# Performance work log

Hardware: AMD Instinct MI355X
Metric: run time of the kernel (lower is better)

Reference implementation:

```python
import jax, jax.numpy as jnp
from jax import lax
import numpy as np

HH = WW = 128          # backbone feature map (2048px image / stride 16)
C_IN = 512
FEAT_STRIDE = 16
N_ANCHOR = 9
NMS_THRESH = 0.7
N_PRE_NMS = 6000
N_POST_NMS = 300
MIN_SIZE = 16
NEG = jnp.float32(-1e30)


def _anchor_base(base_size=16, ratios=(0.5, 1.0, 2.0), scales=(8, 16, 32)):
    py = px = base_size / 2.0
    ab = np.zeros((len(ratios) * len(scales), 4), np.float32)
    for i, r in enumerate(ratios):
        for j, s in enumerate(scales):
            h = base_size * s * np.sqrt(r)
            w = base_size * s * np.sqrt(1.0 / r)
            ab[i * len(scales) + j] = [py - h / 2, px - w / 2, py + h / 2, px + w / 2]
    return ab


def _shifted_anchors(hh, ww):
    # (y1, x1, y2, x2) anchors enumerated row-major over (y, x), anchors innermost
    ab = _anchor_base()
    sy = np.arange(0, hh * FEAT_STRIDE, FEAT_STRIDE, dtype=np.float32)
    sx = np.arange(0, ww * FEAT_STRIDE, FEAT_STRIDE, dtype=np.float32)
    sx, sy = np.meshgrid(sx, sy)
    shift = np.stack((sy.ravel(), sx.ravel(), sy.ravel(), sx.ravel()), axis=1)
    anc = (ab[None, :, :] + shift[:, None, :]).reshape(-1, 4)
    return jnp.asarray(anc)


def _conv(x, w, b):
    y = lax.conv_general_dilated(x, w, (1, 1), 'SAME',
                                 dimension_numbers=('NHWC', 'HWIO', 'NHWC'))
    return y + b


def _loc2bbox(anchor, loc):
    sh = anchor[:, 2] - anchor[:, 0]
    sw = anchor[:, 3] - anchor[:, 1]
    scy = anchor[:, 0] + 0.5 * sh
    scx = anchor[:, 1] + 0.5 * sw
    cy = loc[:, 0] * sh + scy
    cx = loc[:, 1] * sw + scx
    h = jnp.exp(loc[:, 2]) * sh
    w = jnp.exp(loc[:, 3]) * sw
    return jnp.stack([cy - 0.5 * h, cx - 0.5 * w, cy + 0.5 * h, cx + 0.5 * w], axis=1)


def _nms(boxes, scores, thresh, n_out):
    # Greedy NMS with a fixed output size; invalid slots are zeroed.
    y1, x1, y2, x2 = boxes[:, 0], boxes[:, 1], boxes[:, 2], boxes[:, 3]
    areas = (y2 - y1) * (x2 - x1)

    def step(valid, _):
        s = jnp.where(valid, scores, NEG)
        i = jnp.argmax(s)
        ok = s[i] > NEG
        iy1 = jnp.maximum(y1, y1[i]); ix1 = jnp.maximum(x1, x1[i])
        iy2 = jnp.minimum(y2, y2[i]); ix2 = jnp.minimum(x2, x2[i])
        inter = jnp.maximum(iy2 - iy1, 0.0) * jnp.maximum(ix2 - ix1, 0.0)
        iou = inter / (areas + areas[i] - inter + 1e-9)
        valid = valid & (iou <= thresh)  # picked box suppresses itself (iou=1)
        return valid, (i, ok)

    _, (idx, oks) = lax.scan(step, jnp.ones(scores.shape, bool), None, length=n_out)
    return boxes[idx] * oks[:, None].astype(boxes.dtype)


def _proposals(loc, fg_score, anchor, img_h, img_w, scale):
    dst = _loc2bbox(anchor, loc)
    dst = jnp.stack([jnp.clip(dst[:, 0], 0.0, img_h),
                     jnp.clip(dst[:, 1], 0.0, img_w),
                     jnp.clip(dst[:, 2], 0.0, img_h),
                     jnp.clip(dst[:, 3], 0.0, img_w)], axis=1)
    min_size = MIN_SIZE * scale
    hs = dst[:, 2] - dst[:, 0]
    ws = dst[:, 3] - dst[:, 1]
    keep = (hs >= min_size) & (ws >= min_size)
    sc = jnp.where(keep, fg_score, -jnp.inf)
    top_s, top_i = lax.top_k(sc, N_PRE_NMS)
    return _nms(dst[top_i], top_s, NMS_THRESH, N_POST_NMS)


def _rpn_forward(x, conv_w, conv_b, loc_w, loc_b, score_w, score_b, img_h, img_w, scale):
    n, hh, ww, _ = x.shape
    anchor = _shifted_anchors(hh, ww)                    # [hh*ww*9, 4]
    h = jax.nn.relu(_conv(x, conv_w, conv_b))            # [n, hh, ww, 512]
    rpn_loc = _conv(h, loc_w, loc_b).reshape(n, -1, 4)   # [n, hh*ww*9, 4]
    rpn_score_map = _conv(h, score_w, score_b)           # [n, hh, ww, 18]
    soft = jax.nn.softmax(rpn_score_map.reshape(n, hh, ww, N_ANCHOR, 2), axis=-1)
    rpn_fg = soft[..., 1].reshape(n, -1)                 # [n, hh*ww*9]
    rpn_score = rpn_score_map.reshape(n, -1, 2)
    roi = _proposals(rpn_loc[0], rpn_fg[0], anchor, img_h, img_w, scale)  # [300, 4]
    return rpn_loc, rpn_score, roi, anchor


def setup_inputs() -> dict:
    key = jax.random.key(0)
    ks = jax.random.split(key, 4)
    return {
        "x": jax.random.normal(ks[0], (1, HH, WW, C_IN), jnp.float32),
        "conv_w": jax.random.normal(ks[1], (3, 3, C_IN, 512), jnp.float32) * 0.02,
        "conv_b": jnp.zeros((512,), jnp.float32),
        "loc_w": jax.random.normal(ks[2], (1, 1, 512, 36), jnp.float32) * 0.02,
        "loc_b": jnp.zeros((36,), jnp.float32),
        "score_w": jax.random.normal(ks[3], (1, 1, 512, 18), jnp.float32) * 0.02,
        "score_b": jnp.zeros((18,), jnp.float32),
        "img_h": HH * FEAT_STRIDE,
        "img_w": WW * FEAT_STRIDE,
        "scale": 1,
    }


def reference(x, conv_w, conv_b, loc_w, loc_b, score_w, score_b, img_h, img_w, scale):
    return _rpn_forward(x, conv_w, conv_b, loc_w, loc_b, score_w, score_b,
                        float(img_h), float(img_w), float(scale))
```

## Files before the change

### kernel.cpp

```cpp
#include <hip/hip_runtime.h>
#include <math.h>

typedef unsigned int u32;
typedef unsigned long long u64;
typedef _Float16 half8 __attribute__((ext_vector_type(8)));
typedef float f32x4 __attribute__((ext_vector_type(4)));

#define N_PIX 16384
#define N_ANC 147456
#define N_PRE 6000
#define TIE_BASE 6144
#define TIE_CAP  16384

#define OFF_H      0ULL
#define OFF_BOXES  33554432ULL
#define OFF_KEYS   35913728ULL
#define OFF_W54    36503552ULL
#define OFF_B54    36634624ULL
#define OFF_HIST1  36634880ULL
#define OFF_HIST2  36897024ULL
#define OFF_CTRL   37159168ULL
#define OFF_CAND   37159424ULL
#define OFF_SBOX   37339648ULL
#define OFF_MASK   37437952ULL
#define BASE_NEEDED 41961984ULL
#define OFF_XH     41961984ULL
#define OFF_XL     58739200ULL
#define OFF_WHT    75516416ULL
#define OFF_WLT    80235008ULL
#define FULL_NEEDED 84953600ULL

#define KEY_NEGINF 0x007FFFFFu

struct AB { float v[36]; };


__global__ void k_init(u32* hist1, u32* hist2, u32* ctrl, float* roi,
                       float* w54, float* b54,
                       const float* __restrict__ loc_w, const float* __restrict__ loc_b,
                       const float* __restrict__ score_w, const float* __restrict__ score_b) {
  int i = blockIdx.x * blockDim.x + threadIdx.x;
  const int stride = gridDim.x * blockDim.x;
  const int TOT = 65536 * 2 + 64 + 1200 + 32768 + 64;
  for (; i < TOT; i += stride) {
    if (i < 65536) hist1[i] = 0u;
    else if (i < 131072) hist2[i - 65536] = 0u;
    else if (i < 131136) ctrl[i - 131072] = 0u;
    else if (i < 132336) roi[i - 131136] = 0.f;
    else if (i < 165104) {
      int j = i - 132336;
      int k = j >> 6, oc = j & 63;
      float v = 0.f;
      if (oc < 36) v = loc_w[k * 36 + oc];
      else if (oc < 54) v = score_w[k * 18 + oc - 36];
      w54[(((k >> 2) << 6) + oc) * 4 + (k & 3)] = v;
    } else {
      int oc = i - 165104;
      float v = 0.f;
      if (oc < 36) v = loc_b[oc];
      else if (oc < 54) v = score_b[oc - 36];
      b54[oc] = v;
    }
  }
}

__global__ __launch_bounds__(256) void k_split_x(const float* __restrict__ x,
                                                 _Float16* __restrict__ xh,
                                                 _Float16* __restrict__ xl) {
  const int gid = blockIdx.x * blockDim.x + threadIdx.x;
  const int base = gid << 3;
  float a[8];
  *(float4*)&a[0] = *(const float4*)(x + base);
  *(float4*)&a[4] = *(const float4*)(x + base + 4);
  half8 hh, ll;
#pragma unroll
  for (int j = 0; j < 8; ++j) {
    _Float16 hi = (_Float16)a[j];
    hh[j] = hi;
    ll[j] = (_Float16)((a[j] - (float)hi) * 2048.0f);
  }
  *(half8*)(xh + base) = hh;
  *(half8*)(xl + base) = ll;
}

__global__ __launch_bounds__(256) void k_split_w(const float* __restrict__ w,
                                                 _Float16* __restrict__ whT,
                                                 _Float16* __restrict__ wlT) {
  __shared__ _Float16 th[64][72];
  __shared__ _Float16 tl[64][72];
  const int kb = blockIdx.x;
  const int cb = blockIdx.y;
  const int t  = threadIdx.x;
  {
    const int r = t >> 2, cq = t & 3;
    float a[16];
    const float* wp = w + ((size_t)(kb * 64 + r) << 9) + cb * 64 + cq * 16;
#pragma unroll
    for (int j = 0; j < 4; ++j) *(float4*)&a[j << 2] = *(const float4*)(wp + (j << 2));
    half8 h0, h1, l0, l1;
#pragma unroll
    for (int j = 0; j < 8; ++j) {
      _Float16 hi = (_Float16)a[j];
      h0[j] = hi; l0[j] = (_Float16)((a[j] - (float)hi) * 2048.0f);
    }
#pragma unroll
    for (int j = 0; j < 8; ++j) {
      _Float16 hi = (_Float16)a[8 + j];
      h1[j] = hi; l1[j] = (_Float16)((a[8 + j] - (float)hi) * 2048.0f);
    }
    *(half8*)&th[r][cq * 16]     = h0;
    *(half8*)&th[r][cq * 16 + 8] = h1;
    *(half8*)&tl[r][cq * 16]     = l0;
    *(half8*)&tl[r][cq * 16 + 8] = l1;
  }
  __syncthreads();
  {
    const int c = t >> 2, kq = t & 3;
    half8 o0, o1, p0, p1;
#pragma unroll
    for (int j = 0; j < 8; ++j) { o0[j] = th[kq * 16 + j][c];     p0[j] = tl[kq * 16 + j][c]; }
#pragma unroll
    for (int j = 0; j < 8; ++j) { o1[j] = th[kq * 16 + 8 + j][c]; p1[j] = tl[kq * 16 + 8 + j][c]; }
    const size_t dst = (size_t)(cb * 64 + c) * 4608 + kb * 64 + kq * 16;
    *(half8*)(whT + dst)     = o0;
    *(half8*)(whT + dst + 8) = o1;
    *(half8*)(wlT + dst)     = p0;
    *(half8*)(wlT + dst + 8) = p1;
  }
}

#define APAD 40
__global__ __launch_bounds__(256, 2) void k_conv_pre(const _Float16* __restrict__ xh,
                                                     const _Float16* __restrict__ xl,
                                                     const _Float16* __restrict__ whT,
                                                     const _Float16* __restrict__ wlT,
                                                     const float* __restrict__ bias,
                                                     float* __restrict__ h) {
  __shared__ _Float16 Ah[128][APAD];
  __shared__ _Float16 Al[128][APAD];
  __shared__ _Float16 Bh[128][APAD];
  __shared__ _Float16 Bl[128][APAD];

  const int y  = blockIdx.x;
  const int nb = blockIdx.y;
  const int t  = threadIdx.x;
  const int wv = t >> 6, lane = t & 63;
  const int m0 = (wv >> 1) << 6;
  const int n0 = (wv & 1) << 6;
  const int fm = lane & 15;
  const int fq = lane >> 4;

  const int s_m = t >> 1;
  const int s_h = (t & 1) << 4;

  f32x4 acc_hh[4][4];
  f32x4 acc_x[4][4];
#pragma unroll
  for (int i = 0; i < 4; ++i)
#pragma unroll
    for (int j = 0; j < 4; ++j) { acc_hh[i][j] = (f32x4)0.f; acc_x[i][j] = (f32x4)0.f; }

#pragma unroll 1
  for (int kb = 0; kb < 144; ++kb) {
    const int tap  = kb >> 4;
    const int ky   = tap / 3, kx = tap - ky * 3;
    const int cin0 = (kb & 15) << 5;

    {
      const int yy = y + ky - 1;
      const int xx = s_m + kx - 1;
      if (yy >= 0 && yy < 128 && xx >= 0 && xx < 128) {
        const size_t off = (((size_t)((yy << 7) + xx)) << 9) + cin0 + s_h;
        *(half8*)&Ah[s_m][s_h]     = *(const half8*)(xh + off);
        *(half8*)&Ah[s_m][s_h + 8] = *(const half8*)(xh + off + 8);
        *(half8*)&Al[s_m][s_h]     = *(const half8*)(xl + off);
        *(half8*)&Al[s_m][s_h + 8] = *(const half8*)(xl + off + 8);
      } else {
        *(half8*)&Ah[s_m][s_h]     = (half8)(_Float16)0;
        *(half8*)&Ah[s_m][s_h + 8] = (half8)(_Float16)0;
        *(half8*)&Al[s_m][s_h]     = (half8)(_Float16)0;
        *(half8*)&Al[s_m][s_h + 8] = (half8)(_Float16)0;
      }
    }
    {
      const size_t off = (size_t)(nb * 128 + s_m) * 4608 + tap * 512 + cin0 + s_h;
      *(half8*)&Bh[s_m][s_h]     = *(const half8*)(whT + off);
      *(half8*)&Bh[s_m][s_h + 8] = *(const half8*)(whT + off + 8);
      *(half8*)&Bl[s_m][s_h]     = *(const half8*)(wlT + off);
      *(half8*)&Bl[s_m][s_h + 8] = *(const half8*)(wlT + off + 8);
    }
    __syncthreads();

    half8 ah[4], al[4], bh[4], bl[4];
#pragma unroll
    for (int i = 0; i < 4; ++i) {
      ah[i] = *(const half8*)&Ah[m0 + (i << 4) + fm][fq << 3];
      al[i] = *(const half8*)&Al[m0 + (i << 4) + fm][fq << 3];
      bh[i] = *(const half8*)&Bh[n0 + (i << 4) + fm][fq << 3];
      bl[i] = *(const half8*)&Bl[n0 + (i << 4) + fm][fq << 3];
    }
#pragma unroll
    for (int mi = 0; mi < 4; ++mi)
#pragma unroll
      for (int ni = 0; ni < 4; ++ni) {
        acc_hh[mi][ni] = __builtin_amdgcn_mfma_f32_16x16x32_f16(ah[mi], bh[ni], acc_hh[mi][ni], 0, 0, 0);
        acc_x[mi][ni]  = __builtin_amdgcn_mfma_f32_16x16x32_f16(ah[mi], bl[ni], acc_x[mi][ni], 0, 0, 0);
        acc_x[mi][ni]  = __builtin_amdgcn_mfma_f32_16x16x32_f16(al[mi], bh[ni], acc_x[mi][ni], 0, 0, 0);
      }
    __syncthreads();
  }

  const float inv2048 = 1.0f / 2048.0f;
#pragma unroll
  for (int mi = 0; mi < 4; ++mi)
#pragma unroll
    for (int ni = 0; ni < 4; ++ni) {
      const int col = n0 + (ni << 4) + fm;
      const float bb = bias[(nb << 7) + col];
#pragma unroll
      for (int r = 0; r < 4; ++r) {
        const int row = m0 + (mi << 4) + (fq << 2) + r;
        float v = acc_hh[mi][ni][r] + acc_x[mi][ni][r] * inv2048 + bb;
        h[(((size_t)((y << 7) + row)) << 9) + (nb << 7) + col] = fmaxf(v, 0.f);
      }
    }
}

__global__ __launch_bounds__(256, 2) void k_conv_fb(const float* __restrict__ x,
                                                    const float* __restrict__ w,
                                                    const float* __restrict__ bias,
                                                    float* __restrict__ h) {
  __shared__ _Float16 Ah[128][APAD];
  __shared__ _Float16 Al[128][APAD];
  __shared__ _Float16 Bh[128][APAD];
  __shared__ _Float16 Bl[128][APAD];

  const int y  = blockIdx.x;
  const int nb = blockIdx.y;
  const int t  = threadIdx.x;
  const int wv = t >> 6, lane = t & 63;
  const int m0 = (wv >> 1) << 6;
  const int n0 = (wv & 1) << 6;
  const int fm = lane & 15;
  const int fq = lane >> 4;
  const int sa_m = t >> 1;
  const int sa_h = (t & 1) << 4;
  const int sb_n = t & 127;
  const int sb_kg = (t >> 7) << 4;

  f32x4 acc_hh[4][4];
  f32x4 acc_x[4][4];
#pragma unroll
  for (int i = 0; i < 4; ++i)
#pragma unroll
    for (int j = 0; j < 4; ++j) { acc_hh[i][j] = (f32x4)0.f; acc_x[i][j] = (f32x4)0.f; }

#pragma unroll 1
  for (int kb = 0; kb < 144; ++kb) {
    const int tap  = kb >> 4;
    const int ky   = tap / 3, kx = tap - ky * 3;
    const int cin0 = (kb & 15) << 5;
    {
      const int yy = y + ky - 1;
      const int xx = sa_m + kx - 1;
      float av[16];
      if (yy >= 0 && yy < 128 && xx >= 0 && xx < 128) {
        const float* ap = x + (((size_t)((yy << 7) + xx)) << 9) + cin0 + sa_h;
#pragma unroll
        for (int j = 0; j < 4; ++j) *(float4*)&av[j << 2] = *(const float4*)(ap + (j << 2));
      } else {
#pragma unroll
        for (int j = 0; j < 16; ++j) av[j] = 0.f;
      }
      half8 h0, h1, l0, l1;
#pragma unroll
      for (int j = 0; j < 8; ++j) {
        _Float16 hi = (_Float16)av[j];
        h0[j] = hi; l0[j] = (_Float16)((av[j] - (float)hi) * 2048.0f);
      }
#pragma unroll
      for (int j = 0; j < 8; ++j) {
        _Float16 hi = (_Float16)av[8 + j];
        h1[j] = hi; l1[j] = (_Float16)((av[8 + j] - (float)hi) * 2048.0f);
      }
      *(half8*)&Ah[sa_m][sa_h]     = h0;
      *(half8*)&Ah[sa_m][sa_h + 8] = h1;
      *(half8*)&Al[sa_m][sa_h]     = l0;
      *(half8*)&Al[sa_m][sa_h + 8] = l1;
    }
    {
      const float* bp = w + ((size_t)(tap * 512 + cin0 + sb_kg) << 9) + (nb << 7) + sb_n;
      float bv[16];
#pragma unroll
      for (int j = 0; j < 16; ++j) bv[j] = bp[(size_t)j << 9];
      half8 h0, h1, l0, l1;
#pragma unroll
      for (int j = 0; j < 8; ++j) {
        _Float16 hi = (_Float16)bv[j];
        h0[j] = hi; l0[j] = (_Float16)((bv[j] - (float)hi) * 2048.0f);
      }
#pragma unroll
      for (int j = 0; j < 8; ++j) {
        _Float16 hi = (_Float16)bv[8 + j];
        h1[j] = hi; l1[j] = (_Float16)((bv[8 + j] - (float)hi) * 2048.0f);
      }
      *(half8*)&Bh[sb_n][sb_kg]     = h0;
      *(half8*)&Bh[sb_n][sb_kg + 8] = h1;
      *(half8*)&Bl[sb_n][sb_kg]     = l0;
      *(half8*)&Bl[sb_n][sb_kg + 8] = l1;
    }
    __syncthreads();
    half8 ah[4], al[4], bh[4], bl[4];
#pragma unroll
    for (int i = 0; i < 4; ++i) {
      ah[i] = *(const half8*)&Ah[m0 + (i << 4) + fm][fq << 3];
      al[i] = *(const half8*)&Al[m0 + (i << 4) + fm][fq << 3];
      bh[i] = *(const half8*)&Bh[n0 + (i << 4) + fm][fq << 3];
      bl[i] = *(const half8*)&Bl[n0 + (i << 4) + fm][fq << 3];
    }
#pragma unroll
    for (int mi = 0; mi < 4; ++mi)
#pragma unroll
      for (int ni = 0; ni < 4; ++ni) {
        acc_hh[mi][ni] = __builtin_amdgcn_mfma_f32_16x16x32_f16(ah[mi], bh[ni], acc_hh[mi][ni], 0, 0, 0);
        acc_x[mi][ni]  = __builtin_amdgcn_mfma_f32_16x16x32_f16(ah[mi], bl[ni], acc_x[mi][ni], 0, 0, 0);
        acc_x[mi][ni]  = __builtin_amdgcn_mfma_f32_16x16x32_f16(al[mi], bh[ni], acc_x[mi][ni], 0, 0, 0);
      }
    __syncthreads();
  }
  const float inv2048 = 1.0f / 2048.0f;
#pragma unroll
  for (int mi = 0; mi < 4; ++mi)
#pragma unroll
    for (int ni = 0; ni < 4; ++ni) {
      const int col = n0 + (ni << 4) + fm;
      const float bb = bias[(nb << 7) + col];
#pragma unroll
      for (int r = 0; r < 4; ++r) {
        const int row = m0 + (mi << 4) + (fq << 2) + r;
        float v = acc_hh[mi][ni][r] + acc_x[mi][ni][r] * inv2048 + bb;
        h[(((size_t)((y << 7) + row)) << 9) + (nb << 7) + col] = fmaxf(v, 0.f);
      }
    }
}

__global__ __launch_bounds__(256) void k_heads(const float* __restrict__ h,
        const float4* __restrict__ w54, const float* __restrict__ b54,
        float* __restrict__ out0, float* __restrict__ out1, float* __restrict__ out3,
        float4* __restrict__ boxes, u32* __restrict__ keys, u32* __restrict__ hist1,
        const int* __restrict__ p_ih, const int* __restrict__ p_iw,
        const int* __restrict__ p_sc, AB ab) {
  __shared__ float hl[16 * 512];
  __shared__ float vals[16][64];
  const int t = threadIdx.x;
  const int wv = t >> 6, lane = t & 63;
  const int pbase = blockIdx.x << 4;

#pragma unroll
  for (int j = 0; j < 8; ++j) {
    const int f = (j << 8) + t;
    ((float4*)hl)[f] = ((const float4*)(h + ((size_t)pbase << 9)))[f];
  }
  __syncthreads();

  const float* hp = hl + ((wv << 2) << 9);
  float a0 = 0.f, a1 = 0.f, a2 = 0.f, a3 = 0.f;
#pragma unroll 4
  for (int kq = 0; kq < 128; ++kq) {
    const float4 wvv = w54[(kq << 6) + lane];
    const float4 h0 = *(const float4*)(hp + (kq << 2));
    const float4 h1 = *(const float4*)(hp + 512 + (kq << 2));
    const float4 h2 = *(const float4*)(hp + 1024 + (kq << 2));
    const float4 h3 = *(const float4*)(hp + 1536 + (kq << 2));
    a0 += h0.x * wvv.x + h0.y * wvv.y + h0.z * wvv.z + h0.w * wvv.w;
    a1 += h1.x * wvv.x + h1.y * wvv.y + h1.z * wvv.z + h1.w * wvv.w;
    a2 += h2.x * wvv.x + h2.y * wvv.y + h2.z * wvv.z + h2.w * wvv.w;
    a3 += h3.x * wvv.x + h3.y * wvv.y + h3.z * wvv.z + h3.w * wvv.w;
  }
  const float bb = b54[lane];
  float av[4] = {a0 + bb, a1 + bb, a2 + bb, a3 + bb};
#pragma unroll
  for (int px = 0; px < 4; ++px) {
    const int p = pbase + (wv << 2) + px;
    vals[(wv << 2) + px][lane] = av[px];
    if (lane < 36) out0[p * 36 + lane] = av[px];
    else if (lane < 54) out1[p * 18 + lane - 36] = av[px];
  }
  __syncthreads();

  if (lane < 36) {
    const int px = lane / 9, a = lane - px * 9;
    const int p = pbase + (wv << 2) + px;
    const float* vv = vals[(wv << 2) + px];
    const float l0 = vv[(a << 2) + 0], l1 = vv[(a << 2) + 1];
    const float l2 = vv[(a << 2) + 2], l3 = vv[(a << 2) + 3];
    const float s0 = vv[36 + (a << 1)], s1 = vv[37 + (a << 1)];
    const int yq = p >> 7, xq = p & 127;
    const float fy = (float)(yq << 4), fx = (float)(xq << 4);
    const float ay1 = ab.v[(a << 2) + 0] + fy;
    const float ax1 = ab.v[(a << 2) + 1] + fx;
    const float ay2 = ab.v[(a << 2) + 2] + fy;
    const float ax2 = ab.v[(a << 2) + 3] + fx;
    const int idx = p * 9 + a;
    *(float4*)(out3 + ((size_t)idx << 2)) = make_float4(ay1, ax1, ay2, ax2);

    const float sh = ay2 - ay1, sw = ax2 - ax1;
    const float scy = ay1 + 0.5f * sh, scx = ax1 + 0.5f * sw;
    const float cy = l0 * sh + scy, cx = l1 * sw + scx;
    const float bh = expf(l2) * sh, bw = expf(l3) * sw;
    const float IH = (float)p_ih[0], IW = (float)p_iw[0];
    float d0 = fminf(fmaxf(cy - 0.5f * bh, 0.f), IH);
    float d1 = fminf(fmaxf(cx - 0.5f * bw, 0.f), IW);
    float d2 = fminf(fmaxf(cy + 0.5f * bh, 0.f), IH);
    float d3 = fminf(fmaxf(cx + 0.5f * bw, 0.f), IW);
    boxes[idx] = make_float4(d0, d1, d2, d3);

    const float minsz = 16.f * (float)p_sc[0];
    const bool keep = (d2 - d0 >= minsz) && (d3 - d1 >= minsz);
    const float mx = fmaxf(s0, s1);
    const float e0 = expf(s0 - mx), e1 = expf(s1 - mx);
    const float fg = e1 / (e0 + e1);
    const float sc = keep ? fg : -INFINITY;
    const u32 u = __float_as_uint(sc);
    const u32 key = (u & 0x80000000u) ? ~u : (u | 0x80000000u);
    keys[idx] = key;
    atomicAdd(&hist1[key >> 16], 1u);
  }
}

__global__ void k_hist2(const u32* __restrict__ keys, const u32* __restrict__ ctrl,
                        u32* __restrict__ hist2) {
  const u32 b1 = ctrl[0];
  int i = blockIdx.x * blockDim.x + threadIdx.x;
  if (i < N_ANC) {
    const u32 k = keys[i];
    if ((k >> 16) == b1) atomicAdd(&hist2[k & 0xFFFFu], 1u);
  }
}

__global__ __launch_bounds__(1024) void k_findcut(const u32* __restrict__ hist,
                                                  u32* __restrict__ ctrl, int mode) {
  __shared__ u32 csum[1024];
  __shared__ u32 suf[1024];
  const int t = threadIdx.x;
  const u32 target = (mode == 0) ? (u32)N_PRE : ((u32)N_PRE - ctrl[1]);
  const int base = t << 6;
  u32 s = 0;
  for (int i = 0; i < 64; ++i) s += hist[base + i];
  csum[t] = s;
  suf[t] = s;
  __syncthreads();
  for (int off = 1; off < 1024; off <<= 1) {
    u32 add = (t + off < 1024) ? suf[t + off] : 0u;
    __syncthreads();
    suf[t] += add;
    __syncthreads();
  }
  const u32 excl = suf[t] - csum[t];
  if (excl < target && target <= suf[t]) {
    u32 cum = excl;
    int bkt = base;
    for (int i = 63; i >= 0; --i) {
      const u32 hh = hist[base + i];
      if (cum < target && target <= cum + hh) { bkt = base + i; break; }
      cum += hh;
    }
    if (mode == 0) { ctrl[0] = (u32)bkt; ctrl[1] = cum; }
    else {
      const u32 Kstar = (ctrl[0] << 16) | (u32)bkt;
      const u32 A = ctrl[1] + cum;
      u32 need = (u32)N_PRE - A;
      if (Kstar == KEY_NEGINF) need = 0u;
      ctrl[2] = Kstar; ctrl[3] = A; ctrl[4] = need;
      ctrl[7] = A + need;
    }
  }
}

__global__ void k_compact(const u32* __restrict__ keys, u32* __restrict__ ctrl,
                          u64* __restrict__ cand) {
  const u32 Kstar = ctrl[2];
  const u32 need  = ctrl[4];
  int i = blockIdx.x * blockDim.x + threadIdx.x;
  if (i >= N_ANC) return;
  const u32 k = keys[i];
  if (k > Kstar) {
    const u32 pos = atomicAdd(&ctrl[5], 1u);
    cand[pos] = ((u64)k << 32) | (u64)(u32)(~(u32)i);
  } else if (k == Kstar && need != 0u) {
    const u32 pos = atomicAdd(&ctrl[6], 1u);
    if (pos < (u32)TIE_CAP) cand[TIE_BASE + pos] = ((u64)Kstar << 32) | (u64)(u32)(~(u32)i);
  }
}

__global__ __launch_bounds__(128) void k_rank(const u32* __restrict__ ctrl,
                                              const u64* __restrict__ cand,
                                              const float4* __restrict__ boxes,
                                              float4* __restrict__ sbox) {
  __shared__ u32 wred[2];
  const u32 A   = ctrl[3];
  const u32 tcc = min(ctrl[6], (u32)TIE_CAP);
  const u32 C   = A + tcc;
  const u32 L   = ctrl[7];
  const u32 i   = blockIdx.x;
  if (i >= C) return;
  const u64 v = (i < A) ? cand[i] : cand[TIE_BASE + (i - A)];
  const int t = threadIdx.x;
  u32 cnt = 0;
  for (u32 j = t; j < A; j += 128) cnt += (cand[j] > v);
  for (u32 j = t; j < tcc; j += 128) cnt += (cand[TIE_BASE + j] > v);
#pragma unroll
  for (int off = 32; off > 0; off >>= 1) cnt += __shfl_xor(cnt, off);
  if ((t & 63) == 0) wred[t >> 6] = cnt;
  __syncthreads();
  if (t == 0) {
    const u32 rank = wred[0] + wred[1];
    if (rank < L) {
      const u32 idx = ~((u32)(v & 0xFFFFFFFFULL));
      sbox[rank] = boxes[idx];
    }
  }
}

__global__ __launch_bounds__(64) void k_mask(const u32* __restrict__ ctrl,
                                             const float4* __restrict__ sbox,
                                             u64* __restrict__ mask) {
  const int L = (int)ctrl[7];
  const int cw = blockIdx.x;
  const int rb = blockIdx.y;
  if (cw < rb) return;
  if (rb * 64 >= L) return;
  const int lane = threadIdx.x;
  const int j = cw * 64 + lane;
  const bool jok = (j < L);
  const float4 cb = jok ? sbox[j] : make_float4(0.f, 0.f, 0.f, 0.f);
  const float careaJ = (cb.z - cb.x) * (cb.w - cb.y);
  const int rbase = rb * 64;
  const float4 rbx = (rbase + lane < L) ? sbox[rbase + lane] : make_float4(0.f, 0.f, 0.f, 0.f);
  const int rmax = min(64, L - rbase);
  for (int r = 0; r < rmax; ++r) {
    const float ry1 = __shfl(rbx.x, r), rx1 = __shfl(rbx.y, r);
    const float ry2 = __shfl(rbx.z, r), rx2 = __shfl(rbx.w, r);
    const float ra = (ry2 - ry1) * (rx2 - rx1);
    const float iy1 = fmaxf(cb.x, ry1), ix1 = fmaxf(cb.y, rx1);
    const float iy2 = fminf(cb.z, ry2), ix2 = fminf(cb.w, rx2);
    const float inter = fmaxf(iy2 - iy1, 0.f) * fmaxf(ix2 - ix1, 0.f);
    const float iou = inter / (careaJ + ra - inter + 1e-9f);
    const bool bit = jok && (iou > 0.7f);
    const u64 bal = __ballot(bit);
    if (lane == 0) mask[(size_t)(rbase + r) * 94 + cw] = bal;
  }
}

__device__ inline u64 valid_mask_fn(int base, int L) {
  const int r = L - base;
  if (r <= 0) return 0ULL;
  if (r >= 64) return ~0ULL;
  return (1ULL << r) - 1ULL;
}
__device__ inline u64 above_mask_fn(int base, int i) {
  if (i < base) return ~0ULL;
  const int s = i - base + 1;
  if (s >= 64) return 0ULL;
  return (~0ULL) << s;
}

__global__ __launch_bounds__(64) void k_greedy(const u32* __restrict__ ctrl,
                                               const float* __restrict__ sboxf,
                                               const u64* __restrict__ mask,
                                               float* __restrict__ roi) {
  const int lane = threadIdx.x;
  const int L = (int)ctrl[7];
  const int base0 = lane << 6;
  const int base1 = (64 + lane) << 6;
  const u64 v0 = valid_mask_fn(base0, L);
  const u64 v1 = (lane < 30) ? valid_mask_fn(base1, L) : 0ULL;
  u64 rem0 = 0ULL, rem1 = 0ULL;
  int i = (L > 0) ? 0 : -1;
  int kept = 0;
  while (i >= 0 && kept < 300) {
    if (lane < 4) roi[kept * 4 + lane] = sboxf[(size_t)i * 4 + lane];
    ++kept;
    rem0 |= mask[(size_t)i * 94 + lane];
    if (lane < 30) rem1 |= mask[(size_t)i * 94 + 64 + lane];
    const u64 f0 = ~rem0 & v0 & above_mask_fn(base0, i);
    const u64 f1 = ~rem1 & v1 & above_mask_fn(base1, i);
    int c0 = f0 ? (base0 + (int)__builtin_ctzll(f0)) : 0x7FFFFFFF;
    int c1 = f1 ? (base1 + (int)__builtin_ctzll(f1)) : 0x7FFFFFFF;
    int c = min(c0, c1);
#pragma unroll
    for (int off = 1; off < 64; off <<= 1) c = min(c, __shfl_xor(c, off));
    i = (c == 0x7FFFFFFF) ? -1 : c;
  }
}

extern "C" void kernel_launch(void* const* d_in, const int* in_sizes, int n_in,
                              void* d_out, int out_size, void* d_ws, size_t ws_size,
                              hipStream_t stream) {
  (void)in_sizes; (void)n_in; (void)out_size;
  if (ws_size < BASE_NEEDED) return;
  const bool fast = (ws_size >= FULL_NEEDED);

  const float* x       = (const float*)d_in[0];
  const float* conv_w  = (const float*)d_in[1];
  const float* conv_b  = (const float*)d_in[2];
  const float* loc_w   = (const float*)d_in[3];
  const float* loc_b   = (const float*)d_in[4];
  const float* score_w = (const float*)d_in[5];
  const float* score_b = (const float*)d_in[6];
  const int* p_ih = (const int*)d_in[7];
  const int* p_iw = (const int*)d_in[8];
  const int* p_sc = (const int*)d_in[9];

  float* out0 = (float*)d_out;
  float* out1 = out0 + 589824;
  float* roi  = out1 + 294912;
  float* out3 = roi + 1200;

  char* ws = (char*)d_ws;
  float*     h     = (float*)(ws + OFF_H);
  float4*    boxes = (float4*)(ws + OFF_BOXES);
  u32*       keys  = (u32*)(ws + OFF_KEYS);
  float*     w54   = (float*)(ws + OFF_W54);
  float*     b54   = (float*)(ws + OFF_B54);
  u32*       hist1 = (u32*)(ws + OFF_HIST1);
  u32*       hist2 = (u32*)(ws + OFF_HIST2);
  u32*       ctrl  = (u32*)(ws + OFF_CTRL);
  u64*       cand  = (u64*)(ws + OFF_CAND);
  float4*    sbox  = (float4*)(ws + OFF_SBOX);
  u64*       mask  = (u64*)(ws + OFF_MASK);
  _Float16*  xh    = (_Float16*)(ws + OFF_XH);
  _Float16*  xl    = (_Float16*)(ws + OFF_XL);
  _Float16*  whT   = (_Float16*)(ws + OFF_WHT);
  _Float16*  wlT   = (_Float16*)(ws + OFF_WLT);

  AB ab;
  {
    const double ratios[3] = {0.5, 1.0, 2.0};
    const double scales[3] = {8.0, 16.0, 32.0};
    for (int i = 0; i < 3; ++i)
      for (int j = 0; j < 3; ++j) {
        const double hh = 16.0 * scales[j] * sqrt(ratios[i]);
        const double wwv = 16.0 * scales[j] * sqrt(1.0 / ratios[i]);
        const int a = i * 3 + j;
        ab.v[a * 4 + 0] = (float)(8.0 - hh / 2.0);
        ab.v[a * 4 + 1] = (float)(8.0 - wwv / 2.0);
        ab.v[a * 4 + 2] = (float)(8.0 + hh / 2.0);
        ab.v[a * 4 + 3] = (float)(8.0 + wwv / 2.0);
      }
  }

  hipLaunchKernelGGL(k_init, dim3(256), dim3(256), 0, stream,
                     hist1, hist2, ctrl, roi, w54, b54, loc_w, loc_b, score_w, score_b);
  if (fast) {
    hipLaunchKernelGGL(k_split_x, dim3(4096), dim3(256), 0, stream, x, xh, xl);
    hipLaunchKernelGGL(k_split_w, dim3(72, 8), dim3(256), 0, stream, conv_w, whT, wlT);
    hipLaunchKernelGGL(k_conv_pre, dim3(128, 4), dim3(256), 0, stream, xh, xl, whT, wlT, conv_b, h);
  } else {
    hipLaunchKernelGGL(k_conv_fb, dim3(128, 4), dim3(256), 0, stream, x, conv_w, conv_b, h);
  }
  hipLaunchKernelGGL(k_heads, dim3(1024), dim3(256), 0, stream,
                     h, (const float4*)w54, b54, out0, out1, out3, boxes, keys, hist1,
                     p_ih, p_iw, p_sc, ab);
  hipLaunchKernelGGL(k_findcut, dim3(1), dim3(1024), 0, stream, hist1, ctrl, 0);
  hipLaunchKernelGGL(k_hist2, dim3(576), dim3(256), 0, stream, keys, ctrl, hist2);
  hipLaunchKernelGGL(k_findcut, dim3(1), dim3(1024), 0, stream, hist2, ctrl, 1);
  hipLaunchKernelGGL(k_compact, dim3(576), dim3(256), 0, stream, keys, ctrl, cand);
  hipLaunchKernelGGL(k_rank, dim3(TIE_BASE + TIE_CAP), dim3(128), 0, stream, ctrl, cand, boxes, sbox);
  hipLaunchKernelGGL(k_mask, dim3(94, 94), dim3(64), 0, stream, ctrl, sbox, mask);
  hipLaunchKernelGGL(k_greedy, dim3(1), dim3(64), 0, stream, ctrl, (const float*)sbox, mask, roi);
}
```

Before: 772.6 us.

## Split conv K across blocks with atomic accumulation and fuse tail kernels

The conv is split into two K halves (grid z=2). Each half atomically adds into h, which a combined prep kernel pre-fills with the bias; ReLU moves into the heads load. Init, split_x and split_w merge into one prep launch. The findcut steps and greedy NMS now run in the last-arriving block of k_heads, k_hist2 and k_mask, removing separate launches. Occupancy is raised to 4 blocks per CU. In exchange it adds float atomics to h (order-dependent rounding) and extra read-modify-write traffic.

```diff
diff --git a/kernel.cpp b/kernel.cpp
--- a/kernel.cpp
+++ b/kernel.cpp
@@ -6,7 +6,6 @@
 typedef _Float16 half8 __attribute__((ext_vector_type(8)));
 typedef float f32x4 __attribute__((ext_vector_type(4)));
 
-#define N_PIX 16384
 #define N_ANC 147456
 #define N_PRE 6000
 #define TIE_BASE 6144
@@ -35,106 +34,118 @@
 struct AB { float v[36]; };
 
 
-__global__ void k_init(u32* hist1, u32* hist2, u32* ctrl, float* roi,
-                       float* w54, float* b54,
-                       const float* __restrict__ loc_w, const float* __restrict__ loc_b,
-                       const float* __restrict__ score_w, const float* __restrict__ score_b) {
-  int i = blockIdx.x * blockDim.x + threadIdx.x;
-  const int stride = gridDim.x * blockDim.x;
-  const int TOT = 65536 * 2 + 64 + 1200 + 32768 + 64;
-  for (; i < TOT; i += stride) {
-    if (i < 65536) hist1[i] = 0u;
-    else if (i < 131072) hist2[i - 65536] = 0u;
-    else if (i < 131136) ctrl[i - 131072] = 0u;
-    else if (i < 132336) roi[i - 131136] = 0.f;
-    else if (i < 165104) {
-      int j = i - 132336;
-      int k = j >> 6, oc = j & 63;
-      float v = 0.f;
-      if (oc < 36) v = loc_w[k * 36 + oc];
-      else if (oc < 54) v = score_w[k * 18 + oc - 36];
-      w54[(((k >> 2) << 6) + oc) * 4 + (k & 3)] = v;
-    } else {
-      int oc = i - 165104;
-      float v = 0.f;
-      if (oc < 36) v = loc_b[oc];
-      else if (oc < 54) v = score_b[oc - 36];
-      b54[oc] = v;
-    }
-  }
-}
-
-__global__ __launch_bounds__(256) void k_split_x(const float* __restrict__ x,
-                                                 _Float16* __restrict__ xh,
-                                                 _Float16* __restrict__ xl) {
-  const int gid = blockIdx.x * blockDim.x + threadIdx.x;
-  const int base = gid << 3;
-  float a[8];
-  *(float4*)&a[0] = *(const float4*)(x + base);
-  *(float4*)&a[4] = *(const float4*)(x + base + 4);
-  half8 hh, ll;
-#pragma unroll
-  for (int j = 0; j < 8; ++j) {
-    _Float16 hi = (_Float16)a[j];
-    hh[j] = hi;
-    ll[j] = (_Float16)((a[j] - (float)hi) * 2048.0f);
-  }
-  *(half8*)(xh + base) = hh;
-  *(half8*)(xl + base) = ll;
-}
-
-__global__ __launch_bounds__(256) void k_split_w(const float* __restrict__ w,
-                                                 _Float16* __restrict__ whT,
-                                                 _Float16* __restrict__ wlT) {
+__global__ __launch_bounds__(256) void k_prep(
+    const float* __restrict__ x, const float* __restrict__ conv_w,
+    const float* __restrict__ conv_b,
+    const float* __restrict__ loc_w, const float* __restrict__ loc_b,
+    const float* __restrict__ score_w, const float* __restrict__ score_b,
+    _Float16* __restrict__ xh, _Float16* __restrict__ xl,
+    _Float16* __restrict__ whT, _Float16* __restrict__ wlT,
+    u32* __restrict__ hist1, u32* __restrict__ hist2, u32* __restrict__ ctrl,
+    float* __restrict__ roi, float* __restrict__ w54, float* __restrict__ b54,
+    float* __restrict__ h, int fast) {
   __shared__ _Float16 th[64][72];
   __shared__ _Float16 tl[64][72];
-  const int kb = blockIdx.x;
-  const int cb = blockIdx.y;
-  const int t  = threadIdx.x;
-  {
-    const int r = t >> 2, cq = t & 3;
-    float a[16];
-    const float* wp = w + ((size_t)(kb * 64 + r) << 9) + cb * 64 + cq * 16;
-#pragma unroll
-    for (int j = 0; j < 4; ++j) *(float4*)&a[j << 2] = *(const float4*)(wp + (j << 2));
-    half8 h0, h1, l0, l1;
+  const int b = blockIdx.x;
+  const int t = threadIdx.x;
+  if (b < 4096) {
+    if (!fast) return;
+    const int base = (b * 256 + t) << 3;
+    float a[8];
+    *(float4*)&a[0] = *(const float4*)(x + base);
+    *(float4*)&a[4] = *(const float4*)(x + base + 4);
+    half8 hh, ll;
 #pragma unroll
     for (int j = 0; j < 8; ++j) {
       _Float16 hi = (_Float16)a[j];
-      h0[j] = hi; l0[j] = (_Float16)((a[j] - (float)hi) * 2048.0f);
-    }
-#pragma unroll
-    for (int j = 0; j < 8; ++j) {
-      _Float16 hi = (_Float16)a[8 + j];
-      h1[j] = hi; l1[j] = (_Float16)((a[8 + j] - (float)hi) * 2048.0f);
-    }
-    *(half8*)&th[r][cq * 16]     = h0;
-    *(half8*)&th[r][cq * 16 + 8] = h1;
-    *(half8*)&tl[r][cq * 16]     = l0;
-    *(half8*)&tl[r][cq * 16 + 8] = l1;
-  }
-  __syncthreads();
-  {
-    const int c = t >> 2, kq = t & 3;
-    half8 o0, o1, p0, p1;
-#pragma unroll
-    for (int j = 0; j < 8; ++j) { o0[j] = th[kq * 16 + j][c];     p0[j] = tl[kq * 16 + j][c]; }
-#pragma unroll
-    for (int j = 0; j < 8; ++j) { o1[j] = th[kq * 16 + 8 + j][c]; p1[j] = tl[kq * 16 + 8 + j][c]; }
-    const size_t dst = (size_t)(cb * 64 + c) * 4608 + kb * 64 + kq * 16;
-    *(half8*)(whT + dst)     = o0;
-    *(half8*)(whT + dst + 8) = o1;
-    *(half8*)(wlT + dst)     = p0;
-    *(half8*)(wlT + dst + 8) = p1;
+      hh[j] = hi;
+      ll[j] = (_Float16)((a[j] - (float)hi) * 2048.0f);
+    }
+    *(half8*)(xh + base) = hh;
+    *(half8*)(xl + base) = ll;
+  } else if (b < 4672) {
+    if (!fast) return;
+    const int idx = b - 4096;
+    const int kb = idx % 72, cb = idx / 72;
+    {
+      const int r = t >> 2, cq = t & 3;
+      float a[16];
+      const float* wp = conv_w + ((size_t)(kb * 64 + r) << 9) + cb * 64 + cq * 16;
+#pragma unroll
+      for (int j = 0; j < 4; ++j) *(float4*)&a[j << 2] = *(const float4*)(wp + (j << 2));
+      half8 h0, h1, l0, l1;
+#pragma unroll
+      for (int j = 0; j < 8; ++j) {
+        _Float16 hi = (_Float16)a[j];
+        h0[j] = hi; l0[j] = (_Float16)((a[j] - (float)hi) * 2048.0f);
+      }
+#pragma unroll
+      for (int j = 0; j < 8; ++j) {
+        _Float16 hi = (_Float16)a[8 + j];
+        h1[j] = hi; l1[j] = (_Float16)((a[8 + j] - (float)hi) * 2048.0f);
+      }
+      *(half8*)&th[r][cq * 16]     = h0;
+      *(half8*)&th[r][cq * 16 + 8] = h1;
+      *(half8*)&tl[r][cq * 16]     = l0;
+      *(half8*)&tl[r][cq * 16 + 8] = l1;
+    }
+    __syncthreads();
+    {
+      const int c = t >> 2, kq = t & 3;
+      half8 o0, o1, p0, p1;
+#pragma unroll
+      for (int j = 0; j < 8; ++j) { o0[j] = th[kq * 16 + j][c];     p0[j] = tl[kq * 16 + j][c]; }
+#pragma unroll
+      for (int j = 0; j < 8; ++j) { o1[j] = th[kq * 16 + 8 + j][c]; p1[j] = tl[kq * 16 + 8 + j][c]; }
+      const size_t dst = (size_t)(cb * 64 + c) * 4608 + kb * 64 + kq * 16;
+      *(half8*)(whT + dst)     = o0;
+      *(half8*)(whT + dst + 8) = o1;
+      *(half8*)(wlT + dst)     = p0;
+      *(half8*)(wlT + dst + 8) = p1;
+    }
+  } else if (b < 4688) {
+    int i = (b - 4672) * 256 + t;
+    const int TOT = 65536 * 2 + 64 + 1200 + 32768 + 64;
+    for (; i < TOT; i += 4096) {
+      if (i < 65536) hist1[i] = 0u;
+      else if (i < 131072) hist2[i - 65536] = 0u;
+      else if (i < 131136) ctrl[i - 131072] = 0u;
+      else if (i < 132336) roi[i - 131136] = 0.f;
+      else if (i < 165104) {
+        int j = i - 132336;
+        int k = j >> 6, oc = j & 63;
+        float v = 0.f;
+        if (oc < 36) v = loc_w[k * 36 + oc];
+        else if (oc < 54) v = score_w[k * 18 + oc - 36];
+        w54[(((k >> 2) << 6) + oc) * 4 + (k & 3)] = v;
+      } else {
+        int oc = i - 165104;
+        float v = 0.f;
+        if (oc < 36) v = loc_b[oc];
+        else if (oc < 54) v = score_b[oc - 36];
+        b54[oc] = v;
+      }
+    }
+  } else {
+    const int blk = b - 4688;
+    const int off = blk * 4096 + t * 16;
+    const int c0 = off & 511;
+    float4 v0 = *(const float4*)(conv_b + c0);
+    float4 v1 = *(const float4*)(conv_b + c0 + 4);
+    float4 v2 = *(const float4*)(conv_b + c0 + 8);
+    float4 v3 = *(const float4*)(conv_b + c0 + 12);
+    *(float4*)(h + off)      = v0;
+    *(float4*)(h + off + 4)  = v1;
+    *(float4*)(h + off + 8)  = v2;
+    *(float4*)(h + off + 12) = v3;
   }
 }
 
 #define APAD 40
-__global__ __launch_bounds__(256, 2) void k_conv_pre(const _Float16* __restrict__ xh,
+__global__ __launch_bounds__(256, 4) void k_conv_pre(const _Float16* __restrict__ xh,
                                                      const _Float16* __restrict__ xl,
                                                      const _Float16* __restrict__ whT,
                                                      const _Float16* __restrict__ wlT,
-                                                     const float* __restrict__ bias,
                                                      float* __restrict__ h) {
   __shared__ _Float16 Ah[128][APAD];
   __shared__ _Float16 Al[128][APAD];
@@ -143,6 +154,7 @@
 
   const int y  = blockIdx.x;
   const int nb = blockIdx.y;
+  const int kh = blockIdx.z;
   const int t  = threadIdx.x;
   const int wv = t >> 6, lane = t & 63;
   const int m0 = (wv >> 1) << 6;
@@ -160,8 +172,9 @@
 #pragma unroll
     for (int j = 0; j < 4; ++j) { acc_hh[i][j] = (f32x4)0.f; acc_x[i][j] = (f32x4)0.f; }
 
+  const int kb0 = kh * 72;
 #pragma unroll 1
-  for (int kb = 0; kb < 144; ++kb) {
+  for (int kb = kb0; kb < kb0 + 72; ++kb) {
     const int tap  = kb >> 4;
     const int ky   = tap / 3, kx = tap - ky * 3;
     const int cin0 = (kb & 15) << 5;
@@ -216,12 +229,11 @@
 #pragma unroll
     for (int ni = 0; ni < 4; ++ni) {
       const int col = n0 + (ni << 4) + fm;
-      const float bb = bias[(nb << 7) + col];
 #pragma unroll
       for (int r = 0; r < 4; ++r) {
         const int row = m0 + (mi << 4) + (fq << 2) + r;
-        float v = acc_hh[mi][ni][r] + acc_x[mi][ni][r] * inv2048 + bb;
-        h[(((size_t)((y << 7) + row)) << 9) + (nb << 7) + col] = fmaxf(v, 0.f);
+        const float v = acc_hh[mi][ni][r] + acc_x[mi][ni][r] * inv2048;
+        unsafeAtomicAdd(&h[(((size_t)((y << 7) + row)) << 9) + (nb << 7) + col], v);
       }
     }
 }
@@ -338,20 +350,60 @@
 #pragma unroll
       for (int r = 0; r < 4; ++r) {
         const int row = m0 + (mi << 4) + (fq << 2) + r;
-        float v = acc_hh[mi][ni][r] + acc_x[mi][ni][r] * inv2048 + bb;
-        h[(((size_t)((y << 7) + row)) << 9) + (nb << 7) + col] = fmaxf(v, 0.f);
-      }
-    }
+        const float v = acc_hh[mi][ni][r] + acc_x[mi][ni][r] * inv2048 + bb;
+        h[(((size_t)((y << 7) + row)) << 9) + (nb << 7) + col] = v;
+      }
+    }
+}
+
+__device__ void findcut_256(const u32* __restrict__ hist, u32* __restrict__ ctrl,
+                            int mode, u32* csum, u32* suf) {
+  const int t = threadIdx.x;
+  const u32 target = (mode == 0) ? (u32)N_PRE : ((u32)N_PRE - ctrl[1]);
+  const int base = t << 8;
+  u32 s = 0;
+  for (int i = 0; i < 256; ++i) s += hist[base + i];
+  csum[t] = s;
+  suf[t] = s;
+  __syncthreads();
+  for (int off = 1; off < 256; off <<= 1) {
+    u32 add = (t + off < 256) ? suf[t + off] : 0u;
+    __syncthreads();
+    suf[t] += add;
+    __syncthreads();
+  }
+  const u32 excl = suf[t] - csum[t];
+  if (excl < target && target <= suf[t]) {
+    u32 cum = excl;
+    int bkt = base;
+    for (int i = 255; i >= 0; --i) {
+      const u32 hh = hist[base + i];
+      if (cum < target && target <= cum + hh) { bkt = base + i; break; }
+      cum += hh;
+    }
+    if (mode == 0) { ctrl[0] = (u32)bkt; ctrl[1] = cum; }
+    else {
+      const u32 Kstar = (ctrl[0] << 16) | (u32)bkt;
+      const u32 A = ctrl[1] + cum;
+      u32 need = (u32)N_PRE - A;
+      if (Kstar == KEY_NEGINF) need = 0u;
+      ctrl[2] = Kstar; ctrl[3] = A; ctrl[4] = need;
+      ctrl[7] = A + need;
+    }
+  }
 }
 
 __global__ __launch_bounds__(256) void k_heads(const float* __restrict__ h,
         const float4* __restrict__ w54, const float* __restrict__ b54,
         float* __restrict__ out0, float* __restrict__ out1, float* __restrict__ out3,
         float4* __restrict__ boxes, u32* __restrict__ keys, u32* __restrict__ hist1,
+        u32* __restrict__ ctrl,
         const int* __restrict__ p_ih, const int* __restrict__ p_iw,
         const int* __restrict__ p_sc, AB ab) {
   __shared__ float hl[16 * 512];
   __shared__ float vals[16][64];
+  __shared__ u32 fc0[256], fc1[256];
+  __shared__ int amlast;
   const int t = threadIdx.x;
   const int wv = t >> 6, lane = t & 63;
   const int pbase = blockIdx.x << 4;
@@ -359,7 +411,10 @@
 #pragma unroll
   for (int j = 0; j < 8; ++j) {
     const int f = (j << 8) + t;
-    ((float4*)hl)[f] = ((const float4*)(h + ((size_t)pbase << 9)))[f];
+    float4 v = ((const float4*)(h + ((size_t)pbase << 9)))[f];
+    v.x = fmaxf(v.x, 0.f); v.y = fmaxf(v.y, 0.f);
+    v.z = fmaxf(v.z, 0.f); v.w = fmaxf(v.w, 0.f);
+    ((float4*)hl)[f] = v;
   }
   __syncthreads();
 
@@ -426,54 +481,36 @@
     keys[idx] = key;
     atomicAdd(&hist1[key >> 16], 1u);
   }
-}
-
-__global__ void k_hist2(const u32* __restrict__ keys, const u32* __restrict__ ctrl,
-                        u32* __restrict__ hist2) {
+  if (t == 0) {
+    __threadfence();
+    amlast = (atomicAdd(&ctrl[8], 1u) == gridDim.x - 1) ? 1 : 0;
+  }
+  __syncthreads();
+  if (amlast) {
+    __threadfence();
+    findcut_256(hist1, ctrl, 0, fc0, fc1);
+  }
+}
+
+__global__ __launch_bounds__(256) void k_hist2(const u32* __restrict__ keys,
+                                               u32* __restrict__ ctrl,
+                                               u32* __restrict__ hist2) {
+  __shared__ u32 fc0[256], fc1[256];
+  __shared__ int amlast;
   const u32 b1 = ctrl[0];
-  int i = blockIdx.x * blockDim.x + threadIdx.x;
+  const int i = blockIdx.x * blockDim.x + threadIdx.x;
   if (i < N_ANC) {
     const u32 k = keys[i];
     if ((k >> 16) == b1) atomicAdd(&hist2[k & 0xFFFFu], 1u);
   }
-}
-
-__global__ __launch_bounds__(1024) void k_findcut(const u32* __restrict__ hist,
-                                                  u32* __restrict__ ctrl, int mode) {
-  __shared__ u32 csum[1024];
-  __shared__ u32 suf[1024];
-  const int t = threadIdx.x;
-  const u32 target = (mode == 0) ? (u32)N_PRE : ((u32)N_PRE - ctrl[1]);
-  const int base = t << 6;
-  u32 s = 0;
-  for (int i = 0; i < 64; ++i) s += hist[base + i];
-  csum[t] = s;
-  suf[t] = s;
+  if (threadIdx.x == 0) {
+    __threadfence();
+    amlast = (atomicAdd(&ctrl[9], 1u) == gridDim.x - 1) ? 1 : 0;
+  }
   __syncthreads();
-  for (int off = 1; off < 1024; off <<= 1) {
-    u32 add = (t + off < 1024) ? suf[t + off] : 0u;
-    __syncthreads();
-    suf[t] += add;
-    __syncthreads();
-  }
-  const u32 excl = suf[t] - csum[t];
-  if (excl < target && target <= suf[t]) {
-    u32 cum = excl;
-    int bkt = base;
-    for (int i = 63; i >= 0; --i) {
-      const u32 hh = hist[base + i];
-      if (cum < target && target <= cum + hh) { bkt = base + i; break; }
-      cum += hh;
-    }
-    if (mode == 0) { ctrl[0] = (u32)bkt; ctrl[1] = cum; }
-    else {
-      const u32 Kstar = (ctrl[0] << 16) | (u32)bkt;
-      const u32 A = ctrl[1] + cum;
-      u32 need = (u32)N_PRE - A;
-      if (Kstar == KEY_NEGINF) need = 0u;
-      ctrl[2] = Kstar; ctrl[3] = A; ctrl[4] = need;
-      ctrl[7] = A + need;
-    }
+  if (amlast) {
+    __threadfence();
+    findcut_256(hist2, ctrl, 1, fc0, fc1);
   }
 }
 
@@ -522,36 +559,6 @@
   }
 }
 
-__global__ __launch_bounds__(64) void k_mask(const u32* __restrict__ ctrl,
-                                             const float4* __restrict__ sbox,
-                                             u64* __restrict__ mask) {
-  const int L = (int)ctrl[7];
-  const int cw = blockIdx.x;
-  const int rb = blockIdx.y;
-  if (cw < rb) return;
-  if (rb * 64 >= L) return;
-  const int lane = threadIdx.x;
-  const int j = cw * 64 + lane;
-  const bool jok = (j < L);
-  const float4 cb = jok ? sbox[j] : make_float4(0.f, 0.f, 0.f, 0.f);
-  const float careaJ = (cb.z - cb.x) * (cb.w - cb.y);
-  const int rbase = rb * 64;
-  const float4 rbx = (rbase + lane < L) ? sbox[rbase + lane] : make_float4(0.f, 0.f, 0.f, 0.f);
-  const int rmax = min(64, L - rbase);
-  for (int r = 0; r < rmax; ++r) {
-    const float ry1 = __shfl(rbx.x, r), rx1 = __shfl(rbx.y, r);
-    const float ry2 = __shfl(rbx.z, r), rx2 = __shfl(rbx.w, r);
-    const float ra = (ry2 - ry1) * (rx2 - rx1);
-    const float iy1 = fmaxf(cb.x, ry1), ix1 = fmaxf(cb.y, rx1);
-    const float iy2 = fminf(cb.z, ry2), ix2 = fminf(cb.w, rx2);
-    const float inter = fmaxf(iy2 - iy1, 0.f) * fmaxf(ix2 - ix1, 0.f);
-    const float iou = inter / (careaJ + ra - inter + 1e-9f);
-    const bool bit = jok && (iou > 0.7f);
-    const u64 bal = __ballot(bit);
-    if (lane == 0) mask[(size_t)(rbase + r) * 94 + cw] = bal;
-  }
-}
-
 __device__ inline u64 valid_mask_fn(int base, int L) {
   const int r = L - base;
   if (r <= 0) return 0ULL;
@@ -565,12 +572,44 @@
   return (~0ULL) << s;
 }
 
-__global__ __launch_bounds__(64) void k_greedy(const u32* __restrict__ ctrl,
-                                               const float* __restrict__ sboxf,
-                                               const u64* __restrict__ mask,
-                                               float* __restrict__ roi) {
+__global__ __launch_bounds__(64) void k_mask(u32* __restrict__ ctrl,
+                                             const float4* __restrict__ sbox,
+                                             u64* __restrict__ mask,
+                                             float* __restrict__ roi) {
+  __shared__ int amlast;
+  const int L = (int)ctrl[7];
+  const int cw = blockIdx.x;
+  const int rb = blockIdx.y;
   const int lane = threadIdx.x;
-  const int L = (int)ctrl[7];
+  if (cw >= rb && rb * 64 < L) {
+    const int j = cw * 64 + lane;
+    const bool jok = (j < L);
+    const float4 cb = jok ? sbox[j] : make_float4(0.f, 0.f, 0.f, 0.f);
+    const float careaJ = (cb.z - cb.x) * (cb.w - cb.y);
+    const int rbase = rb * 64;
+    const float4 rbx = (rbase + lane < L) ? sbox[rbase + lane] : make_float4(0.f, 0.f, 0.f, 0.f);
+    const int rmax = min(64, L - rbase);
+    for (int r = 0; r < rmax; ++r) {
+      const float ry1 = __shfl(rbx.x, r), rx1 = __shfl(rbx.y, r);
+      const float ry2 = __shfl(rbx.z, r), rx2 = __shfl(rbx.w, r);
+      const float ra = (ry2 - ry1) * (rx2 - rx1);
+      const float iy1 = fmaxf(cb.x, ry1), ix1 = fmaxf(cb.y, rx1);
+      const float iy2 = fminf(cb.z, ry2), ix2 = fminf(cb.w, rx2);
+      const float inter = fmaxf(iy2 - iy1, 0.f) * fmaxf(ix2 - ix1, 0.f);
+      const float iou = inter / (careaJ + ra - inter + 1e-9f);
+      const bool bit = jok && (iou > 0.7f);
+      const u64 bal = __ballot(bit);
+      if (lane == 0) mask[(size_t)(rbase + r) * 94 + cw] = bal;
+    }
+  }
+  if (lane == 0) {
+    __threadfence();
+    amlast = (atomicAdd(&ctrl[10], 1u) == gridDim.x * gridDim.y - 1) ? 1 : 0;
+  }
+  __syncthreads();
+  if (!amlast) return;
+  __threadfence();
+  const float* sboxf = (const float*)sbox;
   const int base0 = lane << 6;
   const int base1 = (64 + lane) << 6;
   const u64 v0 = valid_mask_fn(base0, L);
@@ -599,7 +638,7 @@
                               hipStream_t stream) {
   (void)in_sizes; (void)n_in; (void)out_size;
   if (ws_size < BASE_NEEDED) return;
-  const bool fast = (ws_size >= FULL_NEEDED);
+  const int fast = (ws_size >= FULL_NEEDED) ? 1 : 0;
 
   const float* x       = (const float*)d_in[0];
   const float* conv_w  = (const float*)d_in[1];
@@ -650,23 +689,20 @@
       }
   }
 
-  hipLaunchKernelGGL(k_init, dim3(256), dim3(256), 0, stream,
-                     hist1, hist2, ctrl, roi, w54, b54, loc_w, loc_b, score_w, score_b);
+  hipLaunchKernelGGL(k_prep, dim3(6736), dim3(256), 0, stream,
+                     x, conv_w, conv_b, loc_w, loc_b, score_w, score_b,
+                     xh, xl, whT, wlT, hist1, hist2, ctrl, roi, w54, b54, h, fast);
   if (fast) {
-    hipLaunchKernelGGL(k_split_x, dim3(4096), dim3(256), 0, stream, x, xh, xl);
-    hipLaunchKernelGGL(k_split_w, dim3(72, 8), dim3(256), 0, stream, conv_w, whT, wlT);
-    hipLaunchKernelGGL(k_conv_pre, dim3(128, 4), dim3(256), 0, stream, xh, xl, whT, wlT, conv_b, h);
+    hipLaunchKernelGGL(k_conv_pre, dim3(128, 4, 2), dim3(256), 0, stream,
+                       xh, xl, whT, wlT, h);
   } else {
     hipLaunchKernelGGL(k_conv_fb, dim3(128, 4), dim3(256), 0, stream, x, conv_w, conv_b, h);
   }
   hipLaunchKernelGGL(k_heads, dim3(1024), dim3(256), 0, stream,
                      h, (const float4*)w54, b54, out0, out1, out3, boxes, keys, hist1,
-                     p_ih, p_iw, p_sc, ab);
-  hipLaunchKernelGGL(k_findcut, dim3(1), dim3(1024), 0, stream, hist1, ctrl, 0);
+                     ctrl, p_ih, p_iw, p_sc, ab);
   hipLaunchKernelGGL(k_hist2, dim3(576), dim3(256), 0, stream, keys, ctrl, hist2);
-  hipLaunchKernelGGL(k_findcut, dim3(1), dim3(1024), 0, stream, hist2, ctrl, 1);
   hipLaunchKernelGGL(k_compact, dim3(576), dim3(256), 0, stream, keys, ctrl, cand);
   hipLaunchKernelGGL(k_rank, dim3(TIE_BASE + TIE_CAP), dim3(128), 0, stream, ctrl, cand, boxes, sbox);
-  hipLaunchKernelGGL(k_mask, dim3(94, 94), dim3(64), 0, stream, ctrl, sbox, mask);
-  hipLaunchKernelGGL(k_greedy, dim3(1), dim3(64), 0, stream, ctrl, (const float*)sbox, mask, roi);
-}
+  hipLaunchKernelGGL(k_mask, dim3(94, 94), dim3(64), 0, stream, ctrl, sbox, mask, roi);
+}
```

After: 2.360 ms. +205.4%, slower.
